# Kernel optimization log

Hardware: AMD Instinct MI355X
Metric: run time of the kernel (lower is better)

The kernel has to match this reference:

```python
import jax, jax.numpy as jnp
import numpy as np

B, CI, CO, H, W, E, R, K = 32, 128, 256, 64, 64, 8, 16, 3


def setup_inputs() -> dict:
    key = jax.random.key(0)
    ks = jax.random.split(key, 12)
    def n(k, shape, scale):
        return jax.random.normal(k, shape, dtype=jnp.float32) * scale
    return {
        "x": n(ks[0], (B, CI, H, W), 1.0),
        "experts": n(ks[1], (E, CO, CI, K, K), 0.1),
        # routing SE: C -> C/R -> C -> E (1x1 convs == dense on pooled vec)
        "rw1": n(ks[2], (CI // R, CI), 0.05), "rb1": jnp.zeros((CI // R,), jnp.float32),
        "rw2": n(ks[3], (CI, CI // R), 0.05), "rb2": jnp.zeros((CI,), jnp.float32),
        "rw3": n(ks[4], (E, CI), 0.05),      "rb3": jnp.zeros((E,), jnp.float32),
        # channel attention SE on output: CO -> CO/R -> CO
        "aw1": n(ks[5], (CO // R, CO), 0.05), "ab1": jnp.zeros((CO // R,), jnp.float32),
        "aw2": n(ks[6], (CO, CO // R), 0.05), "ab2": jnp.zeros((CO,), jnp.float32),
    }


def reference(x, experts, rw1, rb1, rw2, rb2, rw3, rb3, aw1, ab1, aw2, ab2):
    # --- routing: SE-style gate -> softmax over experts ---
    pooled = x.mean(axis=(2, 3))                       # [B, CI]
    h = jax.nn.relu(pooled @ rw1.T + rb1)              # [B, CI/R]
    s = jax.nn.sigmoid(h @ rw2.T + rb2)                # [B, CI]
    rweights = jax.nn.softmax(s @ rw3.T + rb3, axis=1) # [B, E]
    # --- per-sample expert kernel combination ---
    w = jnp.einsum('be,eoihw->boihw', rweights, experts)  # [B, CO, CI, K, K]
    # --- per-sample conv (== grouped conv with groups=B) via vmap ---
    def conv1(xi, wi):
        # xi: [CI,H,W], wi: [CO,CI,K,K]
        return jax.lax.conv_general_dilated(
            xi[None], wi, window_strides=(1, 1), padding=[(1, 1), (1, 1)],
            dimension_numbers=('NCHW', 'OIHW', 'NCHW'))[0]
    out = jax.vmap(conv1)(x, w)                        # [B, CO, H, W]
    # --- channel attention on output ---
    p = out.mean(axis=(2, 3))                          # [B, CO]
    ca = jax.nn.sigmoid(jax.nn.relu(p @ aw1.T + ab1) @ aw2.T + ab2)
    return out * ca[:, :, None, None]
```

## Files before the change

### kernel.cpp

```cpp
#include <hip/hip_runtime.h>
#include <hip/hip_bf16.h>


#define BB 32
#define CI_ 128
#define CO_ 256
#define HW_ 4096
#define KK 1152

typedef unsigned short u16;
typedef __attribute__((ext_vector_type(8))) __bf16 bf16x8;
typedef __attribute__((ext_vector_type(4))) float floatx4;

typedef const __attribute__((address_space(1))) void* gptr_t;
typedef __attribute__((address_space(3))) void* sptr_t;

__device__ __forceinline__ void gload_lds16(const void* g, void* s) {
  __builtin_amdgcn_global_load_lds((gptr_t)g, (sptr_t)s, 16, 0, 0);
}

__global__ __launch_bounds__(256) void k_prep(const float* __restrict__ x,
                                              u16* __restrict__ xt,
                                              float* __restrict__ Tb,
                                              float* __restrict__ C0a,
                                              float* __restrict__ C63a,
                                              float* __restrict__ R0a,
                                              float* __restrict__ R63a,
                                              float* __restrict__ CNa) {
  int blk = blockIdx.x;
  int b = blk >> 6, y = blk & 63;
  __shared__ u16 ts[64][132];
  int tid = threadIdx.x;
  const float* xb = x + ((size_t)b << 19) + (y << 6);
#pragma unroll
  for (int it = 0; it < 8; it++) {
    int idx = it * 256 + tid;
    int ci = idx >> 4, x4 = idx & 15;
    float4 v = *(const float4*)(xb + (size_t)ci * 4096 + x4 * 4);
    float rs = v.x + v.y + v.z + v.w;
    rs += __shfl_xor(rs, 1); rs += __shfl_xor(rs, 2);
    rs += __shfl_xor(rs, 4); rs += __shfl_xor(rs, 8);
    float ce = __shfl(v.w, 15, 16);
    if (x4 == 0) {
      int o = b * 128 + ci;
      atomicAdd(&Tb[o], rs);
      atomicAdd(&C0a[o], v.x);
      atomicAdd(&C63a[o], ce);
      if (y == 0)  { R0a[o]  = rs; CNa[o * 4 + 0] = v.x; CNa[o * 4 + 1] = ce; }
      if (y == 63) { R63a[o] = rs; CNa[o * 4 + 2] = v.x; CNa[o * 4 + 3] = ce; }
    }
    __hip_bfloat16 h0 = __float2bfloat16(v.x), h1 = __float2bfloat16(v.y);
    __hip_bfloat16 h2 = __float2bfloat16(v.z), h3 = __float2bfloat16(v.w);
    int xx = x4 << 2;
    ts[xx + 0][ci] = *(const u16*)&h0;
    ts[xx + 1][ci] = *(const u16*)&h1;
    ts[xx + 2][ci] = *(const u16*)&h2;
    ts[xx + 3][ci] = *(const u16*)&h3;
  }
  __syncthreads();
  uint2* ot = (uint2*)(xt + ((size_t)b * HW_ + y * 64) * CI_);
#pragma unroll
  for (int it = 0; it < 8; it++) {
    int o = it * 256 + tid;
    int pix = o >> 5, c4 = o & 31;
    ot[o] = *(const uint2*)&ts[pix][c4 * 4];
  }
}

__global__ __launch_bounds__(128) void k_statsfin(const float* __restrict__ Tb,
    const float* __restrict__ C0a, const float* __restrict__ C63a,
    const float* __restrict__ R0a, const float* __restrict__ R63a,
    const float* __restrict__ CNa,
    float* __restrict__ Sr,
    const float* __restrict__ rw1, const float* __restrict__ rb1,
    const float* __restrict__ rw2, const float* __restrict__ rb2,
    const float* __restrict__ rw3, const float* __restrict__ rb3,
    float* __restrict__ r) {
  int b = blockIdx.x, tid = threadIdx.x;
  int o = b * 128 + tid;
  float T   = Tb[o];
  float r0  = R0a[o],  r63 = R63a[o];
  float c0  = C0a[o],  c63 = C63a[o];
  float cn[4];
  cn[0] = CNa[o * 4 + 0]; cn[1] = CNa[o * 4 + 1];
  cn[2] = CNa[o * 4 + 2]; cn[3] = CNa[o * 4 + 3];
  __shared__ float ps[128], hs[8], ss[128], lg[8];
  ps[tid] = T * (1.0f / 4096.0f);
#pragma unroll
  for (int ky = 0; ky < 3; ky++) {
#pragma unroll
    for (int kx = 0; kx < 3; kx++) {
      int dy = ky - 1, dx = kx - 1;
      float s = T;
      if (dy == -1) s -= r63;
      if (dy ==  1) s -= r0;
      if (dx == -1) s -= c63;
      if (dx ==  1) s -= c0;
      if (dy != 0 && dx != 0) s += cn[(dy == -1 ? 2 : 0) + (dx == -1 ? 1 : 0)];
      Sr[(b * 9 + ky * 3 + kx) * CI_ + tid] = s * (1.0f / 4096.0f);
    }
  }
  __syncthreads();
  int oo = tid >> 4, l = tid & 15;
  {
    float a = 0.f;
#pragma unroll
    for (int j = 0; j < 8; j++) a += ps[l * 8 + j] * rw1[oo * 128 + l * 8 + j];
    a += __shfl_xor(a, 1); a += __shfl_xor(a, 2);
    a += __shfl_xor(a, 4); a += __shfl_xor(a, 8);
    if (l == 0) hs[oo] = fmaxf(a + rb1[oo], 0.f);
  }
  __syncthreads();
  {
    float a = rb2[tid];
#pragma unroll
    for (int j = 0; j < 8; j++) a += hs[j] * rw2[tid * 8 + j];
    ss[tid] = 1.f / (1.f + expf(-a));
  }
  __syncthreads();
  {
    float a = 0.f;
#pragma unroll
    for (int j = 0; j < 8; j++) a += ss[l * 8 + j] * rw3[oo * 128 + l * 8 + j];
    a += __shfl_xor(a, 1); a += __shfl_xor(a, 2);
    a += __shfl_xor(a, 4); a += __shfl_xor(a, 8);
    if (l == 0) lg[oo] = a + rb3[oo];
  }
  __syncthreads();
  if (tid == 0) {
    float m = lg[0];
    for (int e = 1; e < 8; e++) m = fmaxf(m, lg[e]);
    float s = 0.f, ex[8];
    for (int e = 0; e < 8; e++) { ex[e] = expf(lg[e] - m); s += ex[e]; }
    for (int e = 0; e < 8; e++) r[b * 8 + e] = ex[e] / s;
  }
}

__global__ __launch_bounds__(256) void k_combine2(const float* __restrict__ experts,
                                                  const float* __restrict__ r,
                                                  const float* __restrict__ Sr,
                                                  __hip_bfloat16* __restrict__ wr,
                                                  float* __restrict__ p) {
  int co = blockIdx.x & 255, g = blockIdx.x >> 8;
  int tid = threadIdx.x;
  __shared__ float els[8][1152];
  __shared__ float rsh[32][8];
  __shared__ float pw[4];
#pragma unroll
  for (int it = 0; it < 9; it++) {
    int f = it * 256 + tid;
    int e = f / 288, q = f - e * 288;
    float4 ev = *(const float4*)(experts + (size_t)e * 294912 + (size_t)co * 1152 + q * 4);
    *(float4*)&els[e][q * 4] = ev;
  }
  rsh[tid >> 3][tid & 7] = r[tid];
  __syncthreads();
  int s = tid >> 7, ci = tid & 127;
  for (int bb = 0; bb < 4; bb++) {
    int b = g * 8 + bb * 2 + s;
    float rv[8];
#pragma unroll
    for (int e = 0; e < 8; e++) rv[e] = rsh[b][e];
    float pacc = 0.f;
    __hip_bfloat16* wrow = wr + (size_t)(b * 256 + co) * KK;
    const float* sb = Sr + b * KK;
#pragma unroll
    for (int k = 0; k < 9; k++) {
      float v = 0.f;
#pragma unroll
      for (int e = 0; e < 8; e++) v += rv[e] * els[e][ci * 9 + k];
      wrow[k * 128 + ci] = __float2bfloat16(v);
      pacc += v * sb[k * 128 + ci];
    }
    for (int off = 32; off; off >>= 1) pacc += __shfl_down(pacc, off);
    if ((tid & 63) == 0) pw[tid >> 6] = pacc;
    __syncthreads();
    if (ci == 0) p[b * 256 + co] = pw[s * 2] + pw[s * 2 + 1];
    __syncthreads();
  }
}

__global__ __launch_bounds__(256) void k_catt2(const float* __restrict__ p,
    const float* __restrict__ aw1, const float* __restrict__ ab1,
    const float* __restrict__ aw2, const float* __restrict__ ab2,
    float* __restrict__ ca) {
  int b = blockIdx.x, tid = threadIdx.x;
  int o = tid >> 4, l = tid & 15;
  __shared__ float ps[256], ts[16];
  ps[tid] = p[b * 256 + tid];
  __syncthreads();
  {
    float a = 0.f;
#pragma unroll
    for (int j = 0; j < 16; j++) a += ps[l * 16 + j] * aw1[o * 256 + l * 16 + j];
    a += __shfl_xor(a, 1); a += __shfl_xor(a, 2);
    a += __shfl_xor(a, 4); a += __shfl_xor(a, 8);
    if (l == 0) ts[o] = fmaxf(a + ab1[o], 0.f);
  }
  __syncthreads();
  float a = ab2[tid];
#pragma unroll
  for (int j = 0; j < 16; j++) a += ts[j] * aw2[tid * 16 + j];
  ca[b * 256 + tid] = 1.f / (1.f + expf(-a));
}

__global__ __launch_bounds__(256) void k_conv(const u16* __restrict__ xt,
                                              const u16* __restrict__ wr,
                                              const float* __restrict__ ca,
                                              const u16* __restrict__ zp,
                                              float* __restrict__ out) {
  int id = blockIdx.x;
  int b = (id & 7) | (((id >> 9) & 3) << 3);
  int rem = (id >> 3) & 63;
  int coT = rem >> 5, rp = rem & 31;
  int y0 = rp * 2;
  int coBase = coT * 128;
  int tid = threadIdx.x;
  int w = tid >> 6, lane = tid & 63;
  int wm = w & 1, wn = w >> 1;
  int quad = lane >> 4, l15 = lane & 15;
  int cl8 = lane & 7, lr = lane >> 3;

  __shared__ __align__(16) u16 As[128 * 64];
  __shared__ __align__(16) u16 Bs[128 * 64];

  const u16* aP[4];
  int dstO[4], chB[4], ylocB[4], xlocB[4];
#pragma unroll
  for (int ri = 0; ri < 4; ri++) {
    int rr = ri * 32 + w * 8 + lr;
    int c = cl8 ^ (rr & 7);
    aP[ri] = wr + (size_t)(b * 256 + coBase + rr) * KK + c * 8;
    dstO[ri] = rr * 64 + cl8 * 8;
    chB[ri] = c;
    ylocB[ri] = rr >> 6;
    xlocB[ri] = rr & 63;
  }

  int aOff[4][2], bOff[4][2];
#pragma unroll
  for (int i = 0; i < 4; i++) {
    int m = wm * 64 + i * 16 + l15;
    int n = wn * 64 + i * 16 + l15;
#pragma unroll
    for (int h = 0; h < 2; h++) {
      aOff[i][h] = m * 64 + ((((h << 2) | quad) ^ (m & 7)) << 3);
      bOff[i][h] = n * 64 + ((((h << 2) | quad) ^ (n & 7)) << 3);
    }
  }

  floatx4 acc[4][4];
#pragma unroll
  for (int i = 0; i < 4; i++)
#pragma unroll
    for (int j = 0; j < 4; j++) acc[i][j] = floatx4{0.f, 0.f, 0.f, 0.f};

  for (int kidx = 0; kidx < 9; kidx++) {
    int ky = kidx / 3, kx = kidx - ky * 3;
    const u16* bP[4];
    int bStep[4];
#pragma unroll
    for (int ri = 0; ri < 4; ri++) {
      int ys = y0 + ylocB[ri] + ky - 1;
      int xs = xlocB[ri] + kx - 1;
      bool valid = ((unsigned)ys < 64u) && ((unsigned)xs < 64u);
      bP[ri] = valid ? (xt + ((size_t)(b * HW_ + ys * 64 + xs) << 7) + chB[ri] * 8)
                     : (zp + chB[ri] * 8);
      bStep[ri] = valid ? 64 : 0;
    }
#pragma unroll
    for (int cib = 0; cib < 2; cib++) {
      __syncthreads();
#pragma unroll
      for (int ri = 0; ri < 4; ri++)
        gload_lds16(aP[ri] + kidx * 128 + cib * 64, &As[dstO[ri]]);
#pragma unroll
      for (int ri = 0; ri < 4; ri++)
        gload_lds16(bP[ri] + cib * bStep[ri], &Bs[dstO[ri]]);
      __syncthreads();
#pragma unroll
      for (int h = 0; h < 2; h++) {
        bf16x8 af[4], bfv[4];
#pragma unroll
        for (int i = 0; i < 4; i++) af[i] = *(const bf16x8*)&As[aOff[i][h]];
#pragma unroll
        for (int j = 0; j < 4; j++) bfv[j] = *(const bf16x8*)&Bs[bOff[j][h]];
#pragma unroll
        for (int i = 0; i < 4; i++)
#pragma unroll
          for (int j = 0; j < 4; j++)
            acc[i][j] = __builtin_amdgcn_mfma_f32_16x16x32_bf16(af[i], bfv[j], acc[i][j], 0, 0, 0);
      }
    }
  }

  float cav[4][4];
#pragma unroll
  for (int i = 0; i < 4; i++)
#pragma unroll
    for (int ri = 0; ri < 4; ri++)
      cav[i][ri] = ca[b * 256 + coBase + wm * 64 + i * 16 + quad * 4 + ri];
#pragma unroll
  for (int i = 0; i < 4; i++) {
#pragma unroll
    for (int j = 0; j < 4; j++) {
      int n = wn * 64 + j * 16 + l15;
      int yy = y0 + (n >> 6), xx = n & 63;
#pragma unroll
      for (int ri = 0; ri < 4; ri++) {
        int co = coBase + wm * 64 + i * 16 + quad * 4 + ri;
        out[((size_t)(b * 256 + co) << 12) + (yy << 6) + xx] = acc[i][j][ri] * cav[i][ri];
      }
    }
  }
}

extern "C" void kernel_launch(void* const* d_in, const int* in_sizes, int n_in,
                              void* d_out, int out_size, void* d_ws, size_t ws_size,
                              hipStream_t stream) {
  const float* x       = (const float*)d_in[0];
  const float* experts = (const float*)d_in[1];
  const float* rw1 = (const float*)d_in[2];
  const float* rb1 = (const float*)d_in[3];
  const float* rw2 = (const float*)d_in[4];
  const float* rb2 = (const float*)d_in[5];
  const float* rw3 = (const float*)d_in[6];
  const float* rb3 = (const float*)d_in[7];
  const float* aw1 = (const float*)d_in[8];
  const float* ab1 = (const float*)d_in[9];
  const float* aw2 = (const float*)d_in[10];
  const float* ab2 = (const float*)d_in[11];

  char* ws = (char*)d_ws;
  u16*   xt     = (u16*)(ws + 0);
  __hip_bfloat16* wr = (__hip_bfloat16*)(ws + 33554432);
  float* Sr     = (float*)(ws + 52428800);
  float* r      = (float*)(ws + 52592640);
  float* p      = (float*)(ws + 52593664);
  float* ca     = (float*)(ws + 52626432);
  u16*   zp     = (u16*)(ws + 52659200);

  float* Tb   = (float*)(ws + 33554432);
  float* C0a  = Tb + 4096;
  float* C63a = Tb + 8192;
  float* R0a  = Tb + 12288;
  float* R63a = Tb + 16384;
  float* CNa  = Tb + 20480;

  hipMemsetAsync(Tb, 0, 3 * 16384, stream);
  hipMemsetAsync(zp, 0, 256, stream);

  k_prep<<<2048, 256, 0, stream>>>(x, xt, Tb, C0a, C63a, R0a, R63a, CNa);
  k_statsfin<<<32, 128, 0, stream>>>(Tb, C0a, C63a, R0a, R63a, CNa, Sr,
                                     rw1, rb1, rw2, rb2, rw3, rb3, r);
  k_combine2<<<1024, 256, 0, stream>>>(experts, r, Sr, wr, p);
  k_catt2<<<32, 256, 0, stream>>>(p, aw1, ab1, aw2, ab2, ca);
  k_conv<<<2048, 256, 0, stream>>>(xt, (const u16*)wr, ca, zp, (float*)d_out);
}
```

Measured before the change: 313.9 us.

## Double-buffer LDS tiles in conv kernel to overlap loads with MFMA

The conv kernel now keeps two LDS buffers for the A and B tiles. It issues the async global-to-LDS loads for the next channel half or kernel tap before running the MFMAs on the current buffer. This cuts the barriers per k-step from two-per-chunk to one, so memory latency can hide behind compute. In exchange LDS use per block doubles to 64KB, which may lower how many blocks fit on each CU.

Result: no change. 312.2 us (-0.6%).

```diff
diff --git a/kernel.cpp b/kernel.cpp
--- a/kernel.cpp
+++ b/kernel.cpp
@@ -204,11 +204,11 @@
   ca[b * 256 + tid] = 1.f / (1.f + expf(-a));
 }
 
-__global__ __launch_bounds__(256) void k_conv(const u16* __restrict__ xt,
-                                              const u16* __restrict__ wr,
-                                              const float* __restrict__ ca,
-                                              const u16* __restrict__ zp,
-                                              float* __restrict__ out) {
+__global__ __launch_bounds__(256) void k_convd(const u16* __restrict__ xt,
+                                               const u16* __restrict__ wr,
+                                               const float* __restrict__ ca,
+                                               const u16* __restrict__ zp,
+                                               float* __restrict__ out) {
   int id = blockIdx.x;
   int b = (id & 7) | (((id >> 9) & 3) << 3);
   int rem = (id >> 3) & 63;
@@ -221,8 +221,8 @@
   int quad = lane >> 4, l15 = lane & 15;
   int cl8 = lane & 7, lr = lane >> 3;
 
-  __shared__ __align__(16) u16 As[128 * 64];
-  __shared__ __align__(16) u16 Bs[128 * 64];
+  __shared__ __align__(16) u16 As[2 * 8192];
+  __shared__ __align__(16) u16 Bs[2 * 8192];
 
   const u16* aP[4];
   int dstO[4], chB[4], ylocB[4], xlocB[4];
@@ -255,10 +255,11 @@
 #pragma unroll
     for (int j = 0; j < 4; j++) acc[i][j] = floatx4{0.f, 0.f, 0.f, 0.f};
 
-  for (int kidx = 0; kidx < 9; kidx++) {
-    int ky = kidx / 3, kx = kidx - ky * 3;
-    const u16* bP[4];
-    int bStep[4];
+  const u16* bP[4];
+  int bStep[4];
+  auto setBP = [&](int kidx) {
+    int ky = (kidx * 11) >> 5;
+    int kx = kidx - ky * 3;
 #pragma unroll
     for (int ri = 0; ri < 4; ri++) {
       int ys = y0 + ylocB[ri] + ky - 1;
@@ -268,30 +269,52 @@
                      : (zp + chB[ri] * 8);
       bStep[ri] = valid ? 64 : 0;
     }
-#pragma unroll
-    for (int cib = 0; cib < 2; cib++) {
-      __syncthreads();
+  };
+
+  auto compute = [&](int bufC) {
+    int cb = bufC << 13;
+#pragma unroll
+    for (int h = 0; h < 2; h++) {
+      bf16x8 af[4], bfv[4];
+#pragma unroll
+      for (int i = 0; i < 4; i++) af[i] = *(const bf16x8*)&As[cb + aOff[i][h]];
+#pragma unroll
+      for (int j = 0; j < 4; j++) bfv[j] = *(const bf16x8*)&Bs[cb + bOff[j][h]];
+#pragma unroll
+      for (int i = 0; i < 4; i++)
+#pragma unroll
+        for (int j = 0; j < 4; j++)
+          acc[i][j] = __builtin_amdgcn_mfma_f32_16x16x32_bf16(af[i], bfv[j], acc[i][j], 0, 0, 0);
+    }
+  };
+
+  setBP(0);
+#pragma unroll
+  for (int ri = 0; ri < 4; ri++) gload_lds16(aP[ri], &As[dstO[ri]]);
+#pragma unroll
+  for (int ri = 0; ri < 4; ri++) gload_lds16(bP[ri], &Bs[dstO[ri]]);
+  __syncthreads();
+
+  for (int kidx = 0; kidx < 9; kidx++) {
+#pragma unroll
+    for (int ri = 0; ri < 4; ri++)
+      gload_lds16(aP[ri] + kidx * 128 + 64, &As[8192 + dstO[ri]]);
+#pragma unroll
+    for (int ri = 0; ri < 4; ri++)
+      gload_lds16(bP[ri] + bStep[ri], &Bs[8192 + dstO[ri]]);
+    compute(0);
+    __syncthreads();
+    if (kidx < 8) {
+      setBP(kidx + 1);
 #pragma unroll
       for (int ri = 0; ri < 4; ri++)
-        gload_lds16(aP[ri] + kidx * 128 + cib * 64, &As[dstO[ri]]);
+        gload_lds16(aP[ri] + (kidx + 1) * 128, &As[dstO[ri]]);
 #pragma unroll
       for (int ri = 0; ri < 4; ri++)
-        gload_lds16(bP[ri] + cib * bStep[ri], &Bs[dstO[ri]]);
-      __syncthreads();
-#pragma unroll
-      for (int h = 0; h < 2; h++) {
-        bf16x8 af[4], bfv[4];
-#pragma unroll
-        for (int i = 0; i < 4; i++) af[i] = *(const bf16x8*)&As[aOff[i][h]];
-#pragma unroll
-        for (int j = 0; j < 4; j++) bfv[j] = *(const bf16x8*)&Bs[bOff[j][h]];
-#pragma unroll
-        for (int i = 0; i < 4; i++)
-#pragma unroll
-          for (int j = 0; j < 4; j++)
-            acc[i][j] = __builtin_amdgcn_mfma_f32_16x16x32_bf16(af[i], bfv[j], acc[i][j], 0, 0, 0);
-      }
-    }
+        gload_lds16(bP[ri], &Bs[dstO[ri]]);
+    }
+    compute(1);
+    __syncthreads();
   }
 
   float cav[4][4];
@@ -355,5 +378,5 @@
                                      rw1, rb1, rw2, rb2, rw3, rb3, r);
   k_combine2<<<1024, 256, 0, stream>>>(experts, r, Sr, wr, p);
   k_catt2<<<32, 256, 0, stream>>>(p, aw1, ab1, aw2, ab2, ca);
-  k_conv<<<2048, 256, 0, stream>>>(xt, (const u16*)wr, ca, zp, (float*)d_out);
-}
+  k_convd<<<2048, 256, 0, stream>>>(xt, (const u16*)wr, ca, zp, (float*)d_out);
+}
```
